# Performance work log

Hardware: AMD Instinct MI355X
Metric: run time of the kernel (lower is better)

## Reference

```python
import jax, jax.numpy as jnp
import numpy as np

N = 100000      # nodes
E = 3200000     # edges
F_IN = 512      # input features
HID = 16        # hidden (hardcoded in module)
OUT = 1         # out_channels


def setup_inputs() -> dict:
    key = jax.random.key(0)
    k1, k2, k3, k4, k5, k6 = jax.random.split(key, 6)
    x = jax.random.normal(k1, (N, F_IN), dtype=jnp.float32)
    edge_index = jax.random.randint(k2, (2, E), 0, N, dtype=jnp.int32)
    # glorot-ish init for weights, zero bias (PyG GCNConv default: glorot W, zeros b)
    W1 = jax.random.normal(k3, (F_IN, HID), dtype=jnp.float32) * (1.0 / np.sqrt(F_IN))
    b1 = jnp.zeros((HID,), dtype=jnp.float32)
    W2 = jax.random.normal(k4, (HID, OUT), dtype=jnp.float32) * (1.0 / np.sqrt(HID))
    b2 = jnp.zeros((OUT,), dtype=jnp.float32)
    return {"x": x, "W1": W1, "b1": b1, "W2": W2, "b2": b2, "edge_index": edge_index}


def _gcn_conv(x, W, b, src, dst):
    """PyG GCNConv: h = x@W; add self-loops; out_i = sum_j deg_i^-1/2 deg_j^-1/2 h_j + b."""
    h = x @ W  # [N, F_out]
    n = x.shape[0]
    loop = jnp.arange(n, dtype=src.dtype)
    src_sl = jnp.concatenate([src, loop])  # [E+N]
    dst_sl = jnp.concatenate([dst, loop])
    deg = jax.ops.segment_sum(jnp.ones_like(dst_sl, dtype=h.dtype), dst_sl, num_segments=n)
    dinv = jnp.where(deg > 0, jax.lax.rsqrt(deg), 0.0)
    norm = dinv[src_sl] * dinv[dst_sl]  # [E+N]
    msg = h[src_sl] * norm[:, None]     # gather + scale
    out = jax.ops.segment_sum(msg, dst_sl, num_segments=n)  # scatter-add
    return out + b


def reference(x, W1, b1, W2, b2, edge_index):
    src, dst = edge_index[0], edge_index[1]  # flow: source_to_target
    h = jax.nn.relu(_gcn_conv(x, W1, b1, src, dst))
    # dropout(p=0.3) is identity in eval mode
    out = jax.nn.sigmoid(_gcn_conv(h, W2, b2, src, dst))
    return out
```

## Files before the change

### kernel.cpp

```cpp
#include <hip/hip_runtime.h>
#include <math.h>

#define N_NODES 100000
#define N_EDGES 3200000
#define F_IN    512
#define HID     16

#define NBKT     196
#define BKT_NODES 512
#define BKT_CAP  18000
#define BIN_BLOCKS 512
#define CHUNK_E  1024
#define NCHUNKS  (N_EDGES / CHUNK_E)

#define ROWS_PER_CHUNK 8
#define NCHUNK (N_NODES / ROWS_PER_CHUNK)
#define GEMM1_BLOCKS 512

typedef const __attribute__((address_space(1))) void g_void;
typedef __attribute__((address_space(3))) void l_void;

__global__ __launch_bounds__(256)
void k_bin(const int* __restrict__ src, const int* __restrict__ dst,
           int* __restrict__ deg, int* __restrict__ gcur,
           unsigned* __restrict__ bins) {
    __shared__ unsigned stage[NBKT][64];
    __shared__ int cnt[NBKT];
    __shared__ int gb[NBKT];
    const int tid = threadIdx.x;

    for (int c = blockIdx.x; c < NCHUNKS; c += BIN_BLOCKS) {
        for (int b = tid; b < NBKT; b += 256) cnt[b] = 0;
        __syncthreads();
        const int base = c * CHUNK_E;
#pragma unroll
        for (int j = 0; j < 4; ++j) {
            int e = base + j * 256 + tid;
            int d = dst[e];
            int s = src[e];
            atomicAdd(&deg[d], 1);
            int b = d >> 9;
            unsigned w = (unsigned)s | ((unsigned)(d & 511) << 17);
            int p = atomicAdd(&cnt[b], 1);
            if (p < 64) {
                stage[b][p] = w;
            } else {
                int g = atomicAdd(&gcur[b], 1);
                bins[(size_t)b * BKT_CAP + g] = w;
            }
        }
        __syncthreads();
        if (tid < NBKT) {
            int n = cnt[tid]; if (n > 64) n = 64;
            cnt[tid] = n;
            gb[tid] = atomicAdd(&gcur[tid], n);
        }
        __syncthreads();
        const int grp = tid >> 4, ln = tid & 15;
        for (int b = grp; b < NBKT; b += 16) {
            int n = cnt[b], g0 = gb[b];
            for (int j = ln; j < n; j += 16)
                bins[(size_t)b * BKT_CAP + g0 + j] = stage[b][j];
        }
        __syncthreads();
    }
}

__global__ void k_dinv(const int* __restrict__ deg, float* __restrict__ dinv) {
    int i = blockIdx.x * blockDim.x + threadIdx.x;
    if (i < N_NODES) dinv[i] = rsqrtf((float)deg[i] + 1.0f);
}

__global__ __launch_bounds__(256, 2)
void k_gemm1(const float* __restrict__ x, const float* __restrict__ W1,
             const float* __restrict__ dinv, float* __restrict__ hs1) {
    __shared__ float xs[2 * ROWS_PER_CHUNK * F_IN];
    const int tid  = threadIdx.x;
    const int lane = tid & 63;
    const int wib  = tid >> 6;
    const int q    = lane >> 4;
    const int k    = lane & 15;

    float w[128];
    {
        const float* wp = W1 + (size_t)(q * 128) * HID + k;
#pragma unroll
        for (int j = 0; j < 128; ++j) w[j] = wp[(size_t)j * HID];
    }

    int chunk = blockIdx.x;
    int par = 0;
    {
        const float* gb = x + (size_t)chunk * (ROWS_PER_CHUNK * F_IN);
#pragma unroll
        for (int j = 0; j < 4; ++j) {
            int cidx = j * 4 + wib;
            __builtin_amdgcn_global_load_lds(
                (g_void*)(gb + cidx * 256 + lane * 4),
                (l_void*)(xs + cidx * 256), 16, 0, 0);
        }
    }

    for (; chunk < NCHUNK; chunk += GEMM1_BLOCKS) {
        const int nxt = chunk + GEMM1_BLOCKS;
        if (nxt < NCHUNK) {
            const float* gb = x + (size_t)nxt * (ROWS_PER_CHUNK * F_IN);
            float* lb = xs + (par ^ 1) * (ROWS_PER_CHUNK * F_IN);
#pragma unroll
            for (int j = 0; j < 4; ++j) {
                int cidx = j * 4 + wib;
                __builtin_amdgcn_global_load_lds(
                    (g_void*)(gb + cidx * 256 + lane * 4),
                    (l_void*)(lb + cidx * 256), 16, 0, 0);
            }
            asm volatile("s_waitcnt vmcnt(4)" ::: "memory");
        } else {
            asm volatile("s_waitcnt vmcnt(0)" ::: "memory");
        }
        __builtin_amdgcn_sched_barrier(0);
        __builtin_amdgcn_s_barrier();
        __builtin_amdgcn_sched_barrier(0);

        const float* xr0 = xs + par * (ROWS_PER_CHUNK * F_IN) + (wib * 2) * F_IN + q * 128;
        const float* xr1 = xr0 + F_IN;
        float a0 = 0.f, c0 = 0.f, a1 = 0.f, c1 = 0.f;
#pragma unroll
        for (int c = 0; c < 32; ++c) {
            float4 v0 = ((const float4*)xr0)[c];
            float4 v1 = ((const float4*)xr1)[c];
            a0 = fmaf(v0.x, w[4 * c + 0], a0);
            c0 = fmaf(v0.y, w[4 * c + 1], c0);
            a0 = fmaf(v0.z, w[4 * c + 2], a0);
            c0 = fmaf(v0.w, w[4 * c + 3], c0);
            a1 = fmaf(v1.x, w[4 * c + 0], a1);
            c1 = fmaf(v1.y, w[4 * c + 1], c1);
            a1 = fmaf(v1.z, w[4 * c + 2], a1);
            c1 = fmaf(v1.w, w[4 * c + 3], c1);
        }
        float s0 = a0 + c0, s1 = a1 + c1;
        s0 += __shfl_xor(s0, 16);
        s0 += __shfl_xor(s0, 32);
        s1 += __shfl_xor(s1, 16);
        s1 += __shfl_xor(s1, 32);
        const int row = chunk * ROWS_PER_CHUNK + wib * 2;
        if (q == 0) {
            hs1[(size_t)row * HID + k]       = s0 * dinv[row];
            hs1[(size_t)(row + 1) * HID + k] = s1 * dinv[row + 1];
        }
        __builtin_amdgcn_sched_barrier(0);
        __builtin_amdgcn_s_barrier();
        __builtin_amdgcn_sched_barrier(0);
        par ^= 1;
    }
}

__global__ __launch_bounds__(256)
void k_agg1(const unsigned* __restrict__ bins, const int* __restrict__ gcur,
            const float* __restrict__ hs1, float* __restrict__ hsum) {
    __shared__ float acc[BKT_NODES * HID];
    const int b    = blockIdx.x >> 1;
    const int half = blockIdx.x & 1;
    const int tid  = threadIdx.x;
    for (int j = tid; j < BKT_NODES * HID; j += 256) acc[j] = 0.f;
    __syncthreads();

    const int n   = gcur[b];
    const int beg = half ? (n >> 1) : 0;
    const int end = half ? n : (n >> 1);
    const unsigned* wp = bins + (size_t)b * BKT_CAP;
    const int g = tid >> 4, k = tid & 15;
#pragma unroll 8
    for (int i = beg + g; i < end; i += 16) {
        unsigned w = wp[i];
        int s  = w & 0x1FFFF;
        int dl = w >> 17;
        float v = hs1[(size_t)s * HID + k];
        atomicAdd(&acc[dl * HID + k], v);
    }
    __syncthreads();
    float* hb = hsum + (size_t)b * (BKT_NODES * HID);
    for (int j = tid; j < BKT_NODES * HID; j += 256) {
        float v = acc[j];
        if (v != 0.f) atomicAdd(&hb[j], v);
    }
}

__global__ void k_mid(const float* __restrict__ hsum, const float* __restrict__ hs1,
                      const float* __restrict__ dinv, const float* __restrict__ b1,
                      const float* __restrict__ W2, float* __restrict__ ts) {
    int i = blockIdx.x * blockDim.x + threadIdx.x;
    if (i >= N_NODES) return;
    float di = dinv[i];
    const float4* A = (const float4*)(hsum + (size_t)i * HID);
    const float4* H = (const float4*)(hs1  + (size_t)i * HID);
    float t = 0.f;
#pragma unroll
    for (int c = 0; c < 4; ++c) {
        float4 a = A[c];
        float4 h = H[c];
        float z0 = fmaxf((a.x + h.x) * di + b1[4 * c + 0], 0.f);
        float z1 = fmaxf((a.y + h.y) * di + b1[4 * c + 1], 0.f);
        float z2 = fmaxf((a.z + h.z) * di + b1[4 * c + 2], 0.f);
        float z3 = fmaxf((a.w + h.w) * di + b1[4 * c + 3], 0.f);
        t += z0 * W2[4 * c + 0] + z1 * W2[4 * c + 1] + z2 * W2[4 * c + 2] + z3 * W2[4 * c + 3];
    }
    ts[i] = t * di;
}

__global__ __launch_bounds__(256)
void k_agg2fin(const unsigned* __restrict__ bins, const int* __restrict__ gcur,
               const float* __restrict__ ts, const float* __restrict__ dinv,
               const float* __restrict__ b2, float* __restrict__ out) {
    __shared__ float acc[BKT_NODES];
    const int b = blockIdx.x, tid = threadIdx.x;
    for (int j = tid; j < BKT_NODES; j += 256) acc[j] = 0.f;
    __syncthreads();
    const int n = gcur[b];
    const unsigned* wp = bins + (size_t)b * BKT_CAP;
#pragma unroll 8
    for (int i = tid; i < n; i += 256) {
        unsigned w = wp[i];
        atomicAdd(&acc[w >> 17], ts[w & 0x1FFFF]);
    }
    __syncthreads();
    for (int l = tid; l < BKT_NODES; l += 256) {
        int nd = b * BKT_NODES + l;
        if (nd < N_NODES) {
            float z = (ts[nd] + acc[l]) * dinv[nd] + b2[0];
            out[nd] = 1.0f / (1.0f + expf(-z));
        }
    }
}

extern "C" void kernel_launch(void* const* d_in, const int* in_sizes, int n_in,
                              void* d_out, int out_size, void* d_ws, size_t ws_size,
                              hipStream_t stream) {
    const float* x  = (const float*)d_in[0];
    const float* W1 = (const float*)d_in[1];
    const float* b1 = (const float*)d_in[2];
    const float* W2 = (const float*)d_in[3];
    const float* b2 = (const float*)d_in[4];
    const int*   ei = (const int*)d_in[5];
    const int* src = ei;
    const int* dst = ei + N_EDGES;
    float* out = (float*)d_out;

    char* ws = (char*)d_ws;
    float*    hs1  = (float*)ws;
    float*    hsum = hs1 + (size_t)N_NODES * HID;
    int*      deg  = (int*)(hsum + (size_t)NBKT * BKT_NODES * HID);
    int*      gcur = deg + N_NODES;
    float*    dinv = (float*)(gcur + 256);
    float*    ts   = dinv + N_NODES;
    unsigned* bins = (unsigned*)(ts + N_NODES);

    hipMemsetAsync(deg, 0, (N_NODES + 256) * sizeof(int), stream);
    hipMemsetAsync(hsum, 0, (size_t)NBKT * BKT_NODES * HID * sizeof(float), stream);

    k_bin    <<<BIN_BLOCKS, 256, 0, stream>>>(src, dst, deg, gcur, bins);
    k_dinv   <<<(N_NODES + 255) / 256, 256, 0, stream>>>(deg, dinv);
    k_gemm1  <<<GEMM1_BLOCKS, 256, 0, stream>>>(x, W1, dinv, hs1);
    k_agg1   <<<NBKT * 2, 256, 0, stream>>>(bins, gcur, hs1, hsum);
    k_mid    <<<(N_NODES + 255) / 256, 256, 0, stream>>>(hsum, hs1, dinv, b1, W2, ts);
    k_agg2fin<<<NBKT, 256, 0, stream>>>(bins, gcur, ts, dinv, b2, out);
}
```

Measured before the change: 850.0 us.

## Split degree count out of binning, quarter-feature agg1, scatter-based second layer

The degree atomics move out of the binning kernel into a separate edge pass. Layer-1 aggregation now gives each block one bucket and one quarter of the features. It reads the bin entries as uint4 vectors and writes its result straight to hsum, so the hsum memset and the global atomics go away. Layer-2 aggregation drops the per-bucket LDS kernel in favour of global atomic scatter over the raw edges plus a separate finalize kernel. The changes also drop the occupancy hint on gemm1 and reorder the workspace, and they add extra full passes over the edge arrays.

```diff
diff --git a/kernel.cpp b/kernel.cpp
--- a/kernel.cpp
+++ b/kernel.cpp
@@ -20,10 +20,19 @@
 typedef const __attribute__((address_space(1))) void g_void;
 typedef __attribute__((address_space(3))) void l_void;
 
+__global__ void k_deg(const int* __restrict__ dst, int* __restrict__ deg) {
+    int e = blockIdx.x * blockDim.x + threadIdx.x;
+    if (e < N_EDGES) atomicAdd(&deg[dst[e]], 1);
+}
+
+__global__ void k_dinv(const int* __restrict__ deg, float* __restrict__ dinv) {
+    int i = blockIdx.x * blockDim.x + threadIdx.x;
+    if (i < N_NODES) dinv[i] = rsqrtf((float)deg[i] + 1.0f);
+}
+
 __global__ __launch_bounds__(256)
 void k_bin(const int* __restrict__ src, const int* __restrict__ dst,
-           int* __restrict__ deg, int* __restrict__ gcur,
-           unsigned* __restrict__ bins) {
+           int* __restrict__ gcur, unsigned* __restrict__ bins) {
     __shared__ unsigned stage[NBKT][64];
     __shared__ int cnt[NBKT];
     __shared__ int gb[NBKT];
@@ -38,7 +47,6 @@
             int e = base + j * 256 + tid;
             int d = dst[e];
             int s = src[e];
-            atomicAdd(&deg[d], 1);
             int b = d >> 9;
             unsigned w = (unsigned)s | ((unsigned)(d & 511) << 17);
             int p = atomicAdd(&cnt[b], 1);
@@ -66,12 +74,7 @@
     }
 }
 
-__global__ void k_dinv(const int* __restrict__ deg, float* __restrict__ dinv) {
-    int i = blockIdx.x * blockDim.x + threadIdx.x;
-    if (i < N_NODES) dinv[i] = rsqrtf((float)deg[i] + 1.0f);
-}
-
-__global__ __launch_bounds__(256, 2)
+__global__ __launch_bounds__(256)
 void k_gemm1(const float* __restrict__ x, const float* __restrict__ W1,
              const float* __restrict__ dinv, float* __restrict__ hs1) {
     __shared__ float xs[2 * ROWS_PER_CHUNK * F_IN];
@@ -157,37 +160,50 @@
 __global__ __launch_bounds__(256)
 void k_agg1(const unsigned* __restrict__ bins, const int* __restrict__ gcur,
             const float* __restrict__ hs1, float* __restrict__ hsum) {
-    __shared__ float acc[BKT_NODES * HID];
-    const int b    = blockIdx.x >> 1;
-    const int half = blockIdx.x & 1;
-    const int tid  = threadIdx.x;
-    for (int j = tid; j < BKT_NODES * HID; j += 256) acc[j] = 0.f;
+    __shared__ float acc[BKT_NODES * 4];
+    const int b   = blockIdx.x >> 2;
+    const int kq  = blockIdx.x & 3;
+    const int tid = threadIdx.x;
+    for (int j = tid; j < BKT_NODES * 4; j += 256) acc[j] = 0.f;
     __syncthreads();
 
-    const int n   = gcur[b];
-    const int beg = half ? (n >> 1) : 0;
-    const int end = half ? n : (n >> 1);
+    const int n = gcur[b];
     const unsigned* wp = bins + (size_t)b * BKT_CAP;
-    const int g = tid >> 4, k = tid & 15;
-#pragma unroll 8
-    for (int i = beg + g; i < end; i += 16) {
+    const int g  = tid >> 2;
+    const int k3 = tid & 3;
+    const float* hsk = hs1 + kq * 4 + k3;
+
+    int base = 0;
+    for (; base + 256 <= n; base += 256) {
+        const uint4 w = *(const uint4*)(wp + base + g * 4);
+        float v0 = hsk[(size_t)(w.x & 0x1FFFF) * HID];
+        float v1 = hsk[(size_t)(w.y & 0x1FFFF) * HID];
+        float v2 = hsk[(size_t)(w.z & 0x1FFFF) * HID];
+        float v3 = hsk[(size_t)(w.w & 0x1FFFF) * HID];
+        atomicAdd(&acc[(w.x >> 17) * 4 + k3], v0);
+        atomicAdd(&acc[(w.y >> 17) * 4 + k3], v1);
+        atomicAdd(&acc[(w.z >> 17) * 4 + k3], v2);
+        atomicAdd(&acc[(w.w >> 17) * 4 + k3], v3);
+    }
+    for (int i = base + g; i < n; i += 64) {
         unsigned w = wp[i];
-        int s  = w & 0x1FFFF;
-        int dl = w >> 17;
-        float v = hs1[(size_t)s * HID + k];
-        atomicAdd(&acc[dl * HID + k], v);
+        float v = hsk[(size_t)(w & 0x1FFFF) * HID];
+        atomicAdd(&acc[(w >> 17) * 4 + k3], v);
     }
     __syncthreads();
-    float* hb = hsum + (size_t)b * (BKT_NODES * HID);
-    for (int j = tid; j < BKT_NODES * HID; j += 256) {
-        float v = acc[j];
-        if (v != 0.f) atomicAdd(&hb[j], v);
-    }
+
+    float* hb = hsum + (size_t)b * BKT_NODES * HID + kq * 4;
+    int n0 = tid * 2;
+    float4 a0 = *(float4*)&acc[n0 * 4];
+    float4 a1 = *(float4*)&acc[(n0 + 1) * 4];
+    *(float4*)&hb[(size_t)n0 * HID]       = a0;
+    *(float4*)&hb[(size_t)(n0 + 1) * HID] = a1;
 }
 
 __global__ void k_mid(const float* __restrict__ hsum, const float* __restrict__ hs1,
                       const float* __restrict__ dinv, const float* __restrict__ b1,
-                      const float* __restrict__ W2, float* __restrict__ ts) {
+                      const float* __restrict__ W2, float* __restrict__ ts,
+                      float* __restrict__ acc2) {
     int i = blockIdx.x * blockDim.x + threadIdx.x;
     if (i >= N_NODES) return;
     float di = dinv[i];
@@ -204,31 +220,23 @@
         float z3 = fmaxf((a.w + h.w) * di + b1[4 * c + 3], 0.f);
         t += z0 * W2[4 * c + 0] + z1 * W2[4 * c + 1] + z2 * W2[4 * c + 2] + z3 * W2[4 * c + 3];
     }
-    ts[i] = t * di;
-}
-
-__global__ __launch_bounds__(256)
-void k_agg2fin(const unsigned* __restrict__ bins, const int* __restrict__ gcur,
-               const float* __restrict__ ts, const float* __restrict__ dinv,
-               const float* __restrict__ b2, float* __restrict__ out) {
-    __shared__ float acc[BKT_NODES];
-    const int b = blockIdx.x, tid = threadIdx.x;
-    for (int j = tid; j < BKT_NODES; j += 256) acc[j] = 0.f;
-    __syncthreads();
-    const int n = gcur[b];
-    const unsigned* wp = bins + (size_t)b * BKT_CAP;
-#pragma unroll 8
-    for (int i = tid; i < n; i += 256) {
-        unsigned w = wp[i];
-        atomicAdd(&acc[w >> 17], ts[w & 0x1FFFF]);
-    }
-    __syncthreads();
-    for (int l = tid; l < BKT_NODES; l += 256) {
-        int nd = b * BKT_NODES + l;
-        if (nd < N_NODES) {
-            float z = (ts[nd] + acc[l]) * dinv[nd] + b2[0];
-            out[nd] = 1.0f / (1.0f + expf(-z));
-        }
+    float v = t * di;
+    ts[i]   = v;
+    acc2[i] = v;
+}
+
+__global__ void k_scatter2(const int* __restrict__ src, const int* __restrict__ dst,
+                           const float* __restrict__ ts, float* __restrict__ acc2) {
+    int e = blockIdx.x * blockDim.x + threadIdx.x;
+    if (e < N_EDGES) atomicAdd(&acc2[dst[e]], ts[src[e]]);
+}
+
+__global__ void k_fin(const float* __restrict__ acc2, const float* __restrict__ dinv,
+                      const float* __restrict__ b2, float* __restrict__ out) {
+    int i = blockIdx.x * blockDim.x + threadIdx.x;
+    if (i < N_NODES) {
+        float z = acc2[i] * dinv[i] + b2[0];
+        out[i] = 1.0f / (1.0f + expf(-z));
     }
 }
 
@@ -246,21 +254,23 @@
     float* out = (float*)d_out;
 
     char* ws = (char*)d_ws;
-    float*    hs1  = (float*)ws;
+    unsigned* bins = (unsigned*)ws;
+    float*    hs1  = (float*)(bins + (size_t)NBKT * BKT_CAP);
     float*    hsum = hs1 + (size_t)N_NODES * HID;
     int*      deg  = (int*)(hsum + (size_t)NBKT * BKT_NODES * HID);
     int*      gcur = deg + N_NODES;
     float*    dinv = (float*)(gcur + 256);
     float*    ts   = dinv + N_NODES;
-    unsigned* bins = (unsigned*)(ts + N_NODES);
+    float*    acc2 = ts + N_NODES;
 
     hipMemsetAsync(deg, 0, (N_NODES + 256) * sizeof(int), stream);
-    hipMemsetAsync(hsum, 0, (size_t)NBKT * BKT_NODES * HID * sizeof(float), stream);
-
-    k_bin    <<<BIN_BLOCKS, 256, 0, stream>>>(src, dst, deg, gcur, bins);
+
+    k_deg    <<<(N_EDGES + 255) / 256, 256, 0, stream>>>(dst, deg);
     k_dinv   <<<(N_NODES + 255) / 256, 256, 0, stream>>>(deg, dinv);
+    k_bin    <<<BIN_BLOCKS, 256, 0, stream>>>(src, dst, gcur, bins);
     k_gemm1  <<<GEMM1_BLOCKS, 256, 0, stream>>>(x, W1, dinv, hs1);
-    k_agg1   <<<NBKT * 2, 256, 0, stream>>>(bins, gcur, hs1, hsum);
-    k_mid    <<<(N_NODES + 255) / 256, 256, 0, stream>>>(hsum, hs1, dinv, b1, W2, ts);
-    k_agg2fin<<<NBKT, 256, 0, stream>>>(bins, gcur, ts, dinv, b2, out);
-}
+    k_agg1   <<<NBKT * 4, 256, 0, stream>>>(bins, gcur, hs1, hsum);
+    k_mid    <<<(N_NODES + 255) / 256, 256, 0, stream>>>(hsum, hs1, dinv, b1, W2, ts, acc2);
+    k_scatter2<<<(N_EDGES + 255) / 256, 256, 0, stream>>>(src, dst, ts, acc2);
+    k_fin    <<<(N_NODES + 255) / 256, 256, 0, stream>>>(acc2, dinv, b2, out);
+}
```

New measurement: 0.9998 ms. 1.18x slower.
